# Kernel tuning notes

Hardware: AMD Instinct MI355X
Metric: run time of the kernel (lower is better)

The kernel has to match this reference:

```python
import jax, jax.numpy as jnp
import numpy as np

HEADS = 4
OUT_CH = 32
NEG_SLOPE = 0.2  # PyG GATConv default leaky_relu slope


def setup_inputs() -> dict:
    key = jax.random.key(0)
    ks = jax.random.split(key, 8)
    N, E, C_IN = 500000, 1500000, 128
    x = jax.random.normal(ks[0], (N, C_IN), dtype=jnp.float32)
    edge_index = jax.random.randint(ks[1], (2, E), 0, N, dtype=jnp.int64)
    # GATConv params (lin weight, attention vectors, bias)
    W = jax.random.normal(ks[2], (C_IN, HEADS * OUT_CH), dtype=jnp.float32) * (1.0 / np.sqrt(C_IN))
    att_src = jax.random.normal(ks[3], (HEADS, OUT_CH), dtype=jnp.float32) * 0.1
    att_dst = jax.random.normal(ks[4], (HEADS, OUT_CH), dtype=jnp.float32) * 0.1
    bias = jnp.zeros((HEADS * OUT_CH,), dtype=jnp.float32)
    # fc head
    fc_w = jax.random.normal(ks[5], (HEADS * OUT_CH, 1), dtype=jnp.float32) * (1.0 / np.sqrt(HEADS * OUT_CH))
    fc_b = jnp.zeros((1,), dtype=jnp.float32)
    return {"x": x, "edge_index": edge_index, "W": W, "att_src": att_src,
            "att_dst": att_dst, "bias": bias, "fc_w": fc_w, "fc_b": fc_b}


def reference(x, edge_index, W, att_src, att_dst, bias, fc_w, fc_b):
    N = x.shape[0]
    # PyG GATConv adds self-loops by default
    loops = jnp.arange(N, dtype=edge_index.dtype)
    src = jnp.concatenate([edge_index[0], loops])  # [Etot]
    dst = jnp.concatenate([edge_index[1], loops])  # [Etot]

    h = (x @ W).reshape(N, HEADS, OUT_CH)                # [N,H,C]
    a_src = jnp.einsum('nhc,hc->nh', h, att_src)          # [N,H]
    a_dst = jnp.einsum('nhc,hc->nh', h, att_dst)          # [N,H]

    e = a_src[src] + a_dst[dst]                           # [Etot,H]
    e = jax.nn.leaky_relu(e, NEG_SLOPE)
    # segment softmax over incoming edges of each dst node
    e_max = jax.ops.segment_max(e, dst, num_segments=N)   # [N,H]
    e_exp = jnp.exp(e - e_max[dst])
    e_sum = jax.ops.segment_sum(e_exp, dst, num_segments=N)
    alpha = e_exp / e_sum[dst]                            # [Etot,H]

    msg = h[src] * alpha[:, :, None]                      # [Etot,H,C]
    out = jax.ops.segment_sum(msg, dst, num_segments=N)   # [N,H,C]
    out = out.reshape(N, HEADS * OUT_CH) + bias

    out = jax.nn.relu(out)
    logits = out @ fc_w + fc_b                            # [N,1]
    return jax.nn.sigmoid(logits)
```

## Files before the change

### kernel.cpp

```cpp
#include <hip/hip_runtime.h>

typedef __attribute__((ext_vector_type(8))) short bf16x8;
typedef __attribute__((ext_vector_type(4))) float f32x4;

__device__ __forceinline__ unsigned short f2bf(float f){
  unsigned int u = __builtin_bit_cast(unsigned int, f);
  u += 0x7fffu + ((u >> 16) & 1u);
  return (unsigned short)(u >> 16);
}
__device__ __forceinline__ float bf_lo(unsigned int v){
  return __builtin_bit_cast(float, v << 16);
}
__device__ __forceinline__ float bf_hi(unsigned int v){
  return __builtin_bit_cast(float, v & 0xffff0000u);
}
__device__ __forceinline__ float lrelu(float x){ return x > 0.f ? x : 0.2f * x; }

#define GLOAD_LDS16(g, l) \
  __builtin_amdgcn_global_load_lds((const __attribute__((address_space(1))) unsigned int*)(g), \
                                   (__attribute__((address_space(3))) unsigned int*)(l), 16, 0, 0)

__global__ __launch_bounds__(256) void k_zero(int4* __restrict__ p, int n4){
  int i = blockIdx.x * 256 + threadIdx.x;
  if (i < n4){ int4 z; z.x=0; z.y=0; z.z=0; z.w=0; p[i] = z; }
}

__global__ __launch_bounds__(256) void k_wprep(const float* __restrict__ W,
                                               unsigned short* __restrict__ WbfT){
  int i = blockIdx.x * 256 + threadIdx.x;
  int c = i & 127, k = i >> 7;
  WbfT[c * 136 + k] = f2bf(W[k * 128 + c]);
}

__global__ __launch_bounds__(256) void k_gemm(
    const float* __restrict__ x, const unsigned short* __restrict__ WbfT,
    const float* __restrict__ attS, const float* __restrict__ attD,
    unsigned short* __restrict__ h, float* __restrict__ aS, float* __restrict__ aD,
    int N)
{
  __shared__ unsigned short Wt[128][136];
  int tid = threadIdx.x;

  const char* wsrc = (const char*)WbfT;
  #pragma unroll
  for (int it = 0; it < 9; ++it){
    int i = it * 256 + tid;
    if (i < 2176) GLOAD_LDS16(wsrc + (size_t)i * 16, ((char*)Wt) + i * 16);
  }
  __syncthreads();

  int wv = tid >> 6, lane = tid & 63;
  int lrow = lane & 15, lgrp = lane >> 4;

  f32x4 zero; zero[0]=0.f; zero[1]=0.f; zero[2]=0.f; zero[3]=0.f;
  f32x4 acc[2][8];
  #pragma unroll
  for (int rt = 0; rt < 2; ++rt)
    #pragma unroll
    for (int ct = 0; ct < 8; ++ct) acc[rt][ct] = zero;

  int row0b = (int)blockIdx.x * 128 + wv * 32;

  #pragma unroll
  for (int rt = 0; rt < 2; ++rt){
    int row0 = row0b + rt * 16;
    bf16x8 afrag[4];
    #pragma unroll
    for (int kt = 0; kt < 4; ++kt){
      int r = row0 + lrow;
      if (r >= N) r = N - 1;
      const float* xp = x + (size_t)r * 128 + kt * 32 + lgrp * 8;
      f32x4 f0 = *(const f32x4*)xp;
      f32x4 f1 = *(const f32x4*)(xp + 4);
      bf16x8 a;
      #pragma unroll
      for (int j = 0; j < 4; ++j){
        a[j]   = (short)f2bf(f0[j]);
        a[4+j] = (short)f2bf(f1[j]);
      }
      afrag[kt] = a;
    }
    #pragma unroll
    for (int kt = 0; kt < 4; ++kt){
      #pragma unroll
      for (int ct = 0; ct < 8; ++ct){
        bf16x8 b = *(const bf16x8*)&Wt[ct*16 + lrow][kt*32 + lgrp*8];
        acc[rt][ct] = __builtin_amdgcn_mfma_f32_16x16x32_bf16(b, afrag[kt], acc[rt][ct], 0, 0, 0);
      }
    }
  }

  #pragma unroll
  for (int rt = 0; rt < 2; ++rt){
    int row = row0b + rt * 16 + lrow;

    float ps[4] = {0.f,0.f,0.f,0.f}, pd[4] = {0.f,0.f,0.f,0.f};
    #pragma unroll
    for (int ct = 0; ct < 8; ++ct){
      int hh = ct >> 1;
      f32x4 s4 = *(const f32x4*)(attS + ct*16 + lgrp*4);
      f32x4 d4 = *(const f32x4*)(attD + ct*16 + lgrp*4);
      #pragma unroll
      for (int g = 0; g < 4; ++g){
        ps[hh] += acc[rt][ct][g] * s4[g];
        pd[hh] += acc[rt][ct][g] * d4[g];
      }
    }
    #pragma unroll
    for (int hh = 0; hh < 4; ++hh){
      ps[hh] += __shfl_xor(ps[hh], 16, 64);
      ps[hh] += __shfl_xor(ps[hh], 32, 64);
      pd[hh] += __shfl_xor(pd[hh], 16, 64);
      pd[hh] += __shfl_xor(pd[hh], 32, 64);
    }
    if (lgrp == 0 && row < N){
      f32x4 vs, vd;
      #pragma unroll
      for (int hh = 0; hh < 4; ++hh){ vs[hh] = ps[hh]; vd[hh] = pd[hh]; }
      *(f32x4*)(aS + (size_t)row * 4) = vs;
      *(f32x4*)(aD + (size_t)row * 4) = vd;
    }

    if (row < N){
      unsigned short* hp = h + (size_t)row * 128 + lgrp * 4;
      #pragma unroll
      for (int ct = 0; ct < 8; ++ct){
        unsigned int u0 = (unsigned int)f2bf(acc[rt][ct][0])
                        | ((unsigned int)f2bf(acc[rt][ct][1]) << 16);
        unsigned int u1 = (unsigned int)f2bf(acc[rt][ct][2])
                        | ((unsigned int)f2bf(acc[rt][ct][3]) << 16);
        uint2 u; u.x = u0; u.y = u1;
        *(uint2*)(hp + ct * 16) = u;
      }
    }
  }
}

__global__ __launch_bounds__(256) void k_hist(const int* __restrict__ dst, int E,
                                              int* __restrict__ deg){
  int e = blockIdx.x * 256 + threadIdx.x;
  if (e < E) atomicAdd(&deg[dst[e]], 1);
}

__global__ __launch_bounds__(256) void k_chunksum(const int* __restrict__ deg, int N,
                                                  int* __restrict__ bsum){
  __shared__ int sm[256];
  int tid = threadIdx.x;
  int base = blockIdx.x * 2048 + tid * 8;
  int s = 0;
  #pragma unroll
  for (int j = 0; j < 8; ++j) s += (base + j < N) ? deg[base + j] : 0;
  sm[tid] = s; __syncthreads();
  for (int off = 128; off > 0; off >>= 1){
    if (tid < off) sm[tid] += sm[tid + off];
    __syncthreads();
  }
  if (tid == 0) bsum[blockIdx.x] = sm[0];
}

__global__ __launch_bounds__(256) void k_scansums(int* __restrict__ bsum, int nb){
  __shared__ int sm[256];
  int tid = threadIdx.x;
  int carry = 0;
  for (int base = 0; base < nb; base += 256){
    int v = (base + tid < nb) ? bsum[base + tid] : 0;
    sm[tid] = v; __syncthreads();
    for (int off = 1; off < 256; off <<= 1){
      int t = (tid >= off) ? sm[tid - off] : 0;
      __syncthreads();
      sm[tid] += t;
      __syncthreads();
    }
    int incl = sm[tid];
    int total = sm[255];
    __syncthreads();
    if (base + tid < nb) bsum[base + tid] = carry + incl - v;
    carry += total;
  }
}

__global__ __launch_bounds__(256) void k_scanfinal(const int* __restrict__ deg,
    const int* __restrict__ bsum, int N, int E,
    int* __restrict__ rowptr, int* __restrict__ cursor){
  __shared__ int sm[256];
  int tid = threadIdx.x;
  int base = blockIdx.x * 2048 + tid * 8;
  int v[8];
  #pragma unroll
  for (int j = 0; j < 8; ++j) v[j] = (base + j < N) ? deg[base + j] : 0;
  int t = 0;
  #pragma unroll
  for (int j = 0; j < 8; ++j){ int x_ = v[j]; v[j] = t; t += x_; }
  sm[tid] = t; __syncthreads();
  for (int off = 1; off < 256; off <<= 1){
    int u = (tid >= off) ? sm[tid - off] : 0;
    __syncthreads();
    sm[tid] += u;
    __syncthreads();
  }
  int excl = sm[tid] - t;
  int off0 = bsum[blockIdx.x] + excl;
  #pragma unroll
  for (int j = 0; j < 8; ++j){
    if (base + j < N){
      int val = off0 + v[j];
      rowptr[base + j] = val;
      cursor[base + j] = val;
    }
  }
  if (blockIdx.x == 0 && tid == 0) rowptr[N] = E;
}

__global__ __launch_bounds__(256) void k_scatter(const int* __restrict__ src,
    const int* __restrict__ dst, int E, int* __restrict__ cursor,
    int* __restrict__ csr){
  int e = blockIdx.x * 256 + threadIdx.x;
  if (e < E){
    int d = dst[e];
    int p = atomicAdd(&cursor[d], 1);
    csr[p] = src[e];
  }
}

__global__ __launch_bounds__(256) void k_aggr(
    const uint4* __restrict__ h4, const float* __restrict__ aS,
    const float* __restrict__ aD, const int* __restrict__ rowptr,
    const int* __restrict__ csr, const float* __restrict__ bias,
    const float* __restrict__ fcw, const float* __restrict__ fcb,
    float* __restrict__ out, int N)
{
  int lane = threadIdx.x & 63;
  int l16  = lane & 15;
  int node = ((int)blockIdx.x * 256 + (int)threadIdx.x) >> 4;
  if (node >= N) return;
  int head = l16 >> 2;

  float ad    = aD[node * 4 + head];
  float wself = __expf(lrelu(aS[node * 4 + head] + ad));
  float wsum  = wself;

  float acc[8];
  {
    uint4 hv = h4[node * 16 + l16];
    acc[0] = wself * bf_lo(hv.x);  acc[1] = wself * bf_hi(hv.x);
    acc[2] = wself * bf_lo(hv.y);  acc[3] = wself * bf_hi(hv.y);
    acc[4] = wself * bf_lo(hv.z);  acc[5] = wself * bf_hi(hv.z);
    acc[6] = wself * bf_lo(hv.w);  acc[7] = wself * bf_hi(hv.w);
  }

  int rb = rowptr[node], re = rowptr[node + 1];
  for (int j = rb; j < re; j += 4){
    int i1 = (j + 1 < re) ? j + 1 : j;
    int i2 = (j + 2 < re) ? j + 2 : j;
    int i3 = (j + 3 < re) ? j + 3 : j;
    int s0 = csr[j], s1 = csr[i1], s2 = csr[i2], s3 = csr[i3];
    float m1 = (j + 1 < re) ? 1.f : 0.f;
    float m2 = (j + 2 < re) ? 1.f : 0.f;
    float m3 = (j + 3 < re) ? 1.f : 0.f;
    float a0 = aS[s0 * 4 + head];
    float a1 = aS[s1 * 4 + head];
    float a2 = aS[s2 * 4 + head];
    float a3 = aS[s3 * 4 + head];
    uint4 v0 = h4[s0 * 16 + l16];
    uint4 v1 = h4[s1 * 16 + l16];
    uint4 v2 = h4[s2 * 16 + l16];
    uint4 v3 = h4[s3 * 16 + l16];
    float w0 = __expf(lrelu(a0 + ad));
    float w1 = __expf(lrelu(a1 + ad)) * m1;
    float w2 = __expf(lrelu(a2 + ad)) * m2;
    float w3 = __expf(lrelu(a3 + ad)) * m3;
    wsum += w0 + w1 + w2 + w3;
    acc[0] += w0*bf_lo(v0.x) + w1*bf_lo(v1.x) + w2*bf_lo(v2.x) + w3*bf_lo(v3.x);
    acc[1] += w0*bf_hi(v0.x) + w1*bf_hi(v1.x) + w2*bf_hi(v2.x) + w3*bf_hi(v3.x);
    acc[2] += w0*bf_lo(v0.y) + w1*bf_lo(v1.y) + w2*bf_lo(v2.y) + w3*bf_lo(v3.y);
    acc[3] += w0*bf_hi(v0.y) + w1*bf_hi(v1.y) + w2*bf_hi(v2.y) + w3*bf_hi(v3.y);
    acc[4] += w0*bf_lo(v0.z) + w1*bf_lo(v1.z) + w2*bf_lo(v2.z) + w3*bf_lo(v3.z);
    acc[5] += w0*bf_hi(v0.z) + w1*bf_hi(v1.z) + w2*bf_hi(v2.z) + w3*bf_hi(v3.z);
    acc[6] += w0*bf_lo(v0.w) + w1*bf_lo(v1.w) + w2*bf_lo(v2.w) + w3*bf_lo(v3.w);
    acc[7] += w0*bf_hi(v0.w) + w1*bf_hi(v1.w) + w2*bf_hi(v2.w) + w3*bf_hi(v3.w);
  }

  float inv = 1.f / wsum;
  const float* bp = bias + l16 * 8;
  const float* fp = fcw  + l16 * 8;
  f32x4 b0 = *(const f32x4*)bp,      b1 = *(const f32x4*)(bp + 4);
  f32x4 f0 = *(const f32x4*)fp,      f1 = *(const f32x4*)(fp + 4);
  float p = 0.f;
  p += fmaxf(acc[0]*inv + b0[0], 0.f) * f0[0];
  p += fmaxf(acc[1]*inv + b0[1], 0.f) * f0[1];
  p += fmaxf(acc[2]*inv + b0[2], 0.f) * f0[2];
  p += fmaxf(acc[3]*inv + b0[3], 0.f) * f0[3];
  p += fmaxf(acc[4]*inv + b1[0], 0.f) * f1[0];
  p += fmaxf(acc[5]*inv + b1[1], 0.f) * f1[1];
  p += fmaxf(acc[6]*inv + b1[2], 0.f) * f1[2];
  p += fmaxf(acc[7]*inv + b1[3], 0.f) * f1[3];
  #pragma unroll
  for (int m = 1; m < 16; m <<= 1) p += __shfl_xor(p, m, 64);
  if (l16 == 0) out[node] = 1.f / (1.f + __expf(-(p + fcb[0])));
}

extern "C" void kernel_launch(void* const* d_in, const int* in_sizes, int n_in,
                              void* d_out, int out_size, void* d_ws, size_t ws_size,
                              hipStream_t stream) {
  const float* x    = (const float*)d_in[0];
  const int*   ei   = (const int*)  d_in[1];
  const float* W    = (const float*)d_in[2];
  const float* attS = (const float*)d_in[3];
  const float* attD = (const float*)d_in[4];
  const float* bias = (const float*)d_in[5];
  const float* fcw  = (const float*)d_in[6];
  const float* fcb  = (const float*)d_in[7];

  int N = in_sizes[0] / 128;
  int E = in_sizes[1] / 2;
  const int* srcA = ei;
  const int* dstA = ei + E;

  char* ws = (char*)d_ws;
  size_t off = 0;
  auto alloc = [&](size_t bytes) -> void* {
    void* p = ws + off;
    off += (bytes + 255) & ~(size_t)255;
    return p;
  };
  unsigned short* h  = (unsigned short*)alloc((size_t)N * 128 * 2);
  float* aS  = (float*)alloc((size_t)N * 4 * 4);
  float* aD  = (float*)alloc((size_t)N * 4 * 4);
  int* deg    = (int*)alloc((size_t)N * 4);
  int* rowptr = (int*)alloc(((size_t)N + 1) * 4);
  int* cursor = (int*)alloc((size_t)N * 4);
  int* csr    = (int*)alloc((size_t)E * 4);
  int* bsum   = (int*)alloc(4096);
  unsigned short* WbfT = (unsigned short*)alloc(128 * 136 * 2);

  int n4 = (N + 3) / 4;
  k_zero<<<(n4 + 255) / 256, 256, 0, stream>>>((int4*)deg, n4);
  k_wprep<<<64, 256, 0, stream>>>(W, WbfT);
  k_gemm<<<(N + 127) / 128, 256, 0, stream>>>(x, WbfT, attS, attD, h, aS, aD, N);
  k_hist<<<(E + 255) / 256, 256, 0, stream>>>(dstA, E, deg);
  int nb = (N + 2047) / 2048;
  k_chunksum<<<nb, 256, 0, stream>>>(deg, N, bsum);
  k_scansums<<<1, 256, 0, stream>>>(bsum, nb);
  k_scanfinal<<<nb, 256, 0, stream>>>(deg, bsum, N, E, rowptr, cursor);
  k_scatter<<<(E + 255) / 256, 256, 0, stream>>>(srcA, dstA, E, cursor, csr);
  k_aggr<<<(N + 15) / 16, 256, 0, stream>>>((const uint4*)h, aS, aD, rowptr, csr,
                                            bias, fcw, fcb, (float*)d_out, N);
}
```

Baseline: 398.1 us.

## Make GEMM persistent with double-buffered LDS staging of x; merge init kernels

The projection GEMM becomes a persistent kernel with 256 blocks. Each wave walks 16-row slices and double-buffers the fp32 x tiles into LDS via global_load_lds, using an XOR swizzle, so the next slice's load overlaps the current MFMA work. The degree zeroing and W transpose/bf16 conversion are merged into one init kernel to save a launch. This adds 64KB of LDS per block (on top of the ~34KB weight tile), which limits occupancy. A 256-block grid may also underfill the GPU's CUs.

```diff
diff --git a/kernel.cpp b/kernel.cpp
--- a/kernel.cpp
+++ b/kernel.cpp
@@ -20,25 +20,25 @@
   __builtin_amdgcn_global_load_lds((const __attribute__((address_space(1))) unsigned int*)(g), \
                                    (__attribute__((address_space(3))) unsigned int*)(l), 16, 0, 0)
 
-__global__ __launch_bounds__(256) void k_zero(int4* __restrict__ p, int n4){
+__global__ __launch_bounds__(256) void k_init(const float* __restrict__ W,
+                                              unsigned short* __restrict__ WbfT,
+                                              int4* __restrict__ deg4, int n4){
   int i = blockIdx.x * 256 + threadIdx.x;
-  if (i < n4){ int4 z; z.x=0; z.y=0; z.z=0; z.w=0; p[i] = z; }
-}
-
-__global__ __launch_bounds__(256) void k_wprep(const float* __restrict__ W,
-                                               unsigned short* __restrict__ WbfT){
-  int i = blockIdx.x * 256 + threadIdx.x;
-  int c = i & 127, k = i >> 7;
-  WbfT[c * 136 + k] = f2bf(W[k * 128 + c]);
+  if (i < n4){ int4 z; z.x=0; z.y=0; z.z=0; z.w=0; deg4[i] = z; }
+  if (i < 128*128){
+    int c = i & 127, k = i >> 7;
+    WbfT[c * 136 + k] = f2bf(W[k * 128 + c]);
+  }
 }
 
 __global__ __launch_bounds__(256) void k_gemm(
     const float* __restrict__ x, const unsigned short* __restrict__ WbfT,
     const float* __restrict__ attS, const float* __restrict__ attD,
     unsigned short* __restrict__ h, float* __restrict__ aS, float* __restrict__ aD,
-    int N)
+    int N, int nslices)
 {
   __shared__ unsigned short Wt[128][136];
+  __shared__ float xbuf[4][2][16*128];
   int tid = threadIdx.x;
 
   const char* wsrc = (const char*)WbfT;
@@ -52,48 +52,62 @@
   int wv = tid >> 6, lane = tid & 63;
   int lrow = lane & 15, lgrp = lane >> 4;
 
-  f32x4 zero; zero[0]=0.f; zero[1]=0.f; zero[2]=0.f; zero[3]=0.f;
-  f32x4 acc[2][8];
-  #pragma unroll
-  for (int rt = 0; rt < 2; ++rt)
-    #pragma unroll
-    for (int ct = 0; ct < 8; ++ct) acc[rt][ct] = zero;
-
-  int row0b = (int)blockIdx.x * 128 + wv * 32;
-
-  #pragma unroll
-  for (int rt = 0; rt < 2; ++rt){
-    int row0 = row0b + rt * 16;
-    bf16x8 afrag[4];
+  int slice  = (int)blockIdx.x * 4 + wv;
+  int stride = (int)gridDim.x * 4;
+
+  auto STAGE = [&](int s, int b){
+    char* dst0 = (char*)&xbuf[wv][b][0];
+    #pragma unroll
+    for (int k = 0; k < 8; ++k){
+      int c = k * 64 + lane;
+      int r = c >> 5, j = c & 31;
+      int gr = s * 16 + r; if (gr >= N) gr = N - 1;
+      const char* src = (const char*)(x + (size_t)gr * 128) + ((j ^ (r & 7)) << 4);
+      GLOAD_LDS16(src, dst0 + k * 1024);
+    }
+  };
+
+  if (slice < nslices) STAGE(slice, 0);
+  int b = 0;
+
+  for (int s = slice; s < nslices; s += stride){
+    int nx = s + stride;
+    if (nx < nslices){
+      STAGE(nx, b ^ 1);
+      asm volatile("s_waitcnt vmcnt(8)" ::: "memory");
+    } else {
+      asm volatile("s_waitcnt vmcnt(0)" ::: "memory");
+    }
+
+    const f32x4* xb = (const f32x4*)&xbuf[wv][b][0];
+    bf16x8 af[4];
     #pragma unroll
     for (int kt = 0; kt < 4; ++kt){
-      int r = row0 + lrow;
-      if (r >= N) r = N - 1;
-      const float* xp = x + (size_t)r * 128 + kt * 32 + lgrp * 8;
-      f32x4 f0 = *(const f32x4*)xp;
-      f32x4 f1 = *(const f32x4*)(xp + 4);
+      int j0 = kt * 8 + lgrp * 2;
+      f32x4 lo = xb[lrow * 32 + ( j0      ^ (lrow & 7))];
+      f32x4 hi = xb[lrow * 32 + ((j0 + 1) ^ (lrow & 7))];
       bf16x8 a;
       #pragma unroll
       for (int j = 0; j < 4; ++j){
-        a[j]   = (short)f2bf(f0[j]);
-        a[4+j] = (short)f2bf(f1[j]);
+        a[j]   = (short)f2bf(lo[j]);
+        a[4+j] = (short)f2bf(hi[j]);
       }
-      afrag[kt] = a;
-    }
+      af[kt] = a;
+    }
+
+    f32x4 acc[8];
+    #pragma unroll
+    for (int ct = 0; ct < 8; ++ct){ acc[ct][0]=0.f; acc[ct][1]=0.f; acc[ct][2]=0.f; acc[ct][3]=0.f; }
     #pragma unroll
     for (int kt = 0; kt < 4; ++kt){
       #pragma unroll
       for (int ct = 0; ct < 8; ++ct){
-        bf16x8 b = *(const bf16x8*)&Wt[ct*16 + lrow][kt*32 + lgrp*8];
-        acc[rt][ct] = __builtin_amdgcn_mfma_f32_16x16x32_bf16(b, afrag[kt], acc[rt][ct], 0, 0, 0);
+        bf16x8 bw = *(const bf16x8*)&Wt[ct*16 + lrow][kt*32 + lgrp*8];
+        acc[ct] = __builtin_amdgcn_mfma_f32_16x16x32_bf16(bw, af[kt], acc[ct], 0, 0, 0);
       }
     }
-  }
-
-  #pragma unroll
-  for (int rt = 0; rt < 2; ++rt){
-    int row = row0b + rt * 16 + lrow;
-
+
+    int row = s * 16 + lrow;
     float ps[4] = {0.f,0.f,0.f,0.f}, pd[4] = {0.f,0.f,0.f,0.f};
     #pragma unroll
     for (int ct = 0; ct < 8; ++ct){
@@ -102,8 +116,8 @@
       f32x4 d4 = *(const f32x4*)(attD + ct*16 + lgrp*4);
       #pragma unroll
       for (int g = 0; g < 4; ++g){
-        ps[hh] += acc[rt][ct][g] * s4[g];
-        pd[hh] += acc[rt][ct][g] * d4[g];
+        ps[hh] += acc[ct][g] * s4[g];
+        pd[hh] += acc[ct][g] * d4[g];
       }
     }
     #pragma unroll
@@ -120,19 +134,19 @@
       *(f32x4*)(aS + (size_t)row * 4) = vs;
       *(f32x4*)(aD + (size_t)row * 4) = vd;
     }
-
     if (row < N){
       unsigned short* hp = h + (size_t)row * 128 + lgrp * 4;
       #pragma unroll
       for (int ct = 0; ct < 8; ++ct){
-        unsigned int u0 = (unsigned int)f2bf(acc[rt][ct][0])
-                        | ((unsigned int)f2bf(acc[rt][ct][1]) << 16);
-        unsigned int u1 = (unsigned int)f2bf(acc[rt][ct][2])
-                        | ((unsigned int)f2bf(acc[rt][ct][3]) << 16);
+        unsigned int u0 = (unsigned int)f2bf(acc[ct][0])
+                        | ((unsigned int)f2bf(acc[ct][1]) << 16);
+        unsigned int u1 = (unsigned int)f2bf(acc[ct][2])
+                        | ((unsigned int)f2bf(acc[ct][3]) << 16);
         uint2 u; u.x = u0; u.y = u1;
         *(uint2*)(hp + ct * 16) = u;
       }
     }
+    b ^= 1;
   }
 }
 
@@ -334,9 +348,10 @@
   unsigned short* WbfT = (unsigned short*)alloc(128 * 136 * 2);
 
   int n4 = (N + 3) / 4;
-  k_zero<<<(n4 + 255) / 256, 256, 0, stream>>>((int4*)deg, n4);
-  k_wprep<<<64, 256, 0, stream>>>(W, WbfT);
-  k_gemm<<<(N + 127) / 128, 256, 0, stream>>>(x, WbfT, attS, attD, h, aS, aD, N);
+  int ninit = (n4 > 16384) ? n4 : 16384;
+  k_init<<<(ninit + 255) / 256, 256, 0, stream>>>(W, WbfT, (int4*)deg, n4);
+  int nslices = (N + 15) / 16;
+  k_gemm<<<256, 256, 0, stream>>>(x, WbfT, attS, attD, h, aS, aD, N, nslices);
   k_hist<<<(E + 255) / 256, 256, 0, stream>>>(dstA, E, deg);
   int nb = (N + 2047) / 2048;
   k_chunksum<<<nb, 256, 0, stream>>>(deg, N, bsum);
```

New measurement: 384.2 us. -3.5%, faster.
